# Optimization experiments

Measured on AMD Instinct MI355X. Metric: run time of the kernel, lower is better.

The kernel has to match this reference:

```python
import jax, jax.numpy as jnp
import numpy as np
from jax import lax

C = 24        # per-cell state channels
HID = 64      # update MLP hidden width
FIRE_RATE = 0.5
STEPS = 32


def _perception_kernel():
    # identity, sobel-x, sobel-y -> depthwise kernel (3C, 1, 3, 3) in OIHW,
    # tiled C times exactly like torch's kernel.repeat(c,1,1,1) with groups=c.
    ident = np.zeros((3, 3), np.float32); ident[1, 1] = 1.0
    sx = np.array([[-1, 0, 1], [-2, 0, 2], [-1, 0, 1]], np.float32) / 8.0
    sy = sx.T.copy()
    k = np.stack([ident, sx, sy])[:, None, :, :]   # (3, 1, 3, 3)
    return jnp.asarray(np.tile(k, (C, 1, 1, 1)))   # (3C, 1, 3, 3)


def setup_inputs() -> dict:
    key = jax.random.key(0)
    k0, k1, k2, k3 = jax.random.split(key, 4)
    B, H, W = 4, 128, 128
    state = jax.random.normal(k0, (B, C, H, W), jnp.float32)
    # scaled so 32 residual steps stay numerically tame (zero-init in the
    # original is a training trick that would make delta identically 0)
    w1 = jax.random.normal(k1, (HID, 3 * C), jnp.float32) * 0.1
    b1 = jnp.zeros((HID,), jnp.float32)
    w2 = jax.random.normal(k2, (C, HID), jnp.float32) * 0.01
    b2 = jnp.zeros((C,), jnp.float32)
    masks = jax.random.uniform(k3, (STEPS, B, 1, H, W), jnp.float32)
    return {"state": state, "w1": w1, "b1": b1, "w2": w2, "b2": b2, "masks": masks}


def reference(state, w1, b1, w2, b2, masks):
    kernel = _perception_kernel()

    def step(s, m):
        # grouped 3x3 depthwise perception: (B,C,H,W) -> (B,3C,H,W)
        p = lax.conv_general_dilated(
            s, kernel, window_strides=(1, 1), padding="SAME",
            feature_group_count=C,
            dimension_numbers=("NCHW", "OIHW", "NCHW"))
        # 1x1 conv MLP (pointwise, expressed as einsum over channels)
        h = jax.nn.relu(jnp.einsum("bchw,oc->bohw", p, w1) + b1[None, :, None, None])
        delta = jnp.einsum("bchw,oc->bohw", h, w2) + b2[None, :, None, None]
        # stochastic fire: update only cells where uniform < fire_rate
        fire = (m < FIRE_RATE).astype(s.dtype)
        return s + delta * fire, None

    out, _ = lax.scan(step, state, masks)
    return out
```

## Files before the change

### kernel.cpp

```cpp
#include <hip/hip_runtime.h>

typedef __bf16 bf16x8 __attribute__((ext_vector_type(8)));
typedef float  f32x4  __attribute__((ext_vector_type(4)));
typedef float  f32x2  __attribute__((ext_vector_type(2)));

#define NCH 24
#define CP  26
#define HW 128
#define IMG (HW*HW)
#define CHIMG (NCH*IMG)
#define SXP 20
#define SYP 8
#define S1XP 18
#define S1YP 6
#define S1N (S1XP*S1YP)

#define PW1_OFF ((size_t)(4*CHIMG)*4)
#define PW2_OFF (PW1_OFF + 12*64*8*2)
#define PB2_OFF (PW2_OFF + 4*64*8*2)

__global__ void nca_pack_weights(const float* __restrict__ w1, const float* __restrict__ b1,
                                 const float* __restrict__ w2, const float* __restrict__ b2,
                                 char* __restrict__ ws)
{
    short* pw1 = (short*)(ws + PW1_OFF);
    short* pw2 = (short*)(ws + PW2_OFF);
    float* pb2 = (float*)(ws + PB2_OFF);
    const int tid = threadIdx.x;
    for (int idx = tid; idx < 12*64*8; idx += 256) {
        int j  = idx & 7;
        int ll = (idx >> 3) & 63;
        int fs = idx >> 9;
        int m  = fs / 3, s = fs - 3*m;
        int row = m*16 + (ll & 15);
        int kp  = 32*s + 8*(ll >> 4) + j;
        int c = kp >> 2, tt = kp & 3;
        float v;
        if (tt < 3) v = w1[row*72 + 3*c + tt];
        else        v = (c == 0) ? b1[row] : 0.f;
        pw1[idx] = (short)__builtin_bit_cast(unsigned short, (__bf16)v);
    }
    for (int idx = tid; idx < 4*64*8; idx += 256) {
        int j  = idx & 7;
        int ll = (idx >> 3) & 63;
        int fs = idx >> 9;
        int m2 = fs >> 1, s2 = fs & 1;
        int row = m2*16 + (ll & 15);
        int h   = 32*s2 + 8*(ll >> 4) + j;
        float v = (row < 24) ? w2[row*64 + h] : 0.f;
        pw2[idx] = (short)__builtin_bit_cast(unsigned short, (__bf16)v);
    }
    for (int idx = tid; idx < 2*64*4; idx += 256) {
        int r  = idx & 3;
        int ll = (idx >> 2) & 63;
        int m2 = idx >> 8;
        int o  = m2*16 + 4*(ll >> 4) + r;
        pb2[idx] = (o < 24) ? b2[o] : 0.f;
    }
}

template<int XP>
__device__ __forceinline__ void nca_mlp(
    const float* __restrict__ stsrc, int sy, int sx,
    int l, int px, int g, int wv, short (*Hb)[16][72],
    const bf16x8 (&w1r)[12], const short* __restrict__ pw2,
    f32x4& d0, f32x4& d1)
{
    const float* base = stsrc + ((sy-1)*XP + (sx-1))*CP + 2*g;
    bf16x8 pf[3];
    #pragma unroll
    for (int s = 0; s < 3; ++s) {
        #define LDV(dy,dx) (*(const f32x2*)(base + ((dy)*XP + (dx))*CP + 8*s))
        f32x2 v00=LDV(0,0), v01=LDV(0,1), v02=LDV(0,2);
        f32x2 v10=LDV(1,0), v11=LDV(1,1), v12=LDV(1,2);
        f32x2 v20=LDV(2,0), v21=LDV(2,1), v22=LDV(2,2);
        #undef LDV
        f32x2 gx = (v02 - v00 + 2.f*(v12 - v10) + (v22 - v20)) * 0.125f;
        f32x2 gy = (v20 - v00 + 2.f*(v21 - v01) + (v22 - v02)) * 0.125f;
        pf[s][0] = (__bf16)v11.x;
        pf[s][1] = (__bf16)gx.x;
        pf[s][2] = (__bf16)gy.x;
        pf[s][3] = (__bf16)((s == 0 && g == 0) ? 1.f : 0.f);
        pf[s][4] = (__bf16)v11.y;
        pf[s][5] = (__bf16)gx.y;
        pf[s][6] = (__bf16)gy.y;
        pf[s][7] = (__bf16)0.f;
    }

    f32x4 acc1[4] = {};
    #pragma unroll
    for (int m = 0; m < 4; ++m) {
        #pragma unroll
        for (int s = 0; s < 3; ++s) {
            acc1[m] = __builtin_amdgcn_mfma_f32_16x16x32_bf16(w1r[m*3 + s], pf[s], acc1[m], 0, 0, 0);
        }
    }

    #pragma unroll
    for (int m = 0; m < 4; ++m) {
        unsigned int b0 = __builtin_bit_cast(unsigned short, (__bf16)fmaxf(acc1[m][0], 0.f));
        unsigned int b1_ = __builtin_bit_cast(unsigned short, (__bf16)fmaxf(acc1[m][1], 0.f));
        unsigned int b2_ = __builtin_bit_cast(unsigned short, (__bf16)fmaxf(acc1[m][2], 0.f));
        unsigned int b3 = __builtin_bit_cast(unsigned short, (__bf16)fmaxf(acc1[m][3], 0.f));
        uint2 w; w.x = b0 | (b1_ << 16); w.y = b2_ | (b3 << 16);
        *(uint2*)&Hb[wv][px][m*16 + 4*g] = w;
    }

    f32x4 acc2[2] = {};
    #pragma unroll
    for (int s2 = 0; s2 < 2; ++s2) {
        bf16x8 hv = *(const bf16x8*)&Hb[wv][px][8*g + 32*s2];
        #pragma unroll
        for (int m2 = 0; m2 < 2; ++m2) {
            bf16x8 a2 = *(const bf16x8*)&pw2[((m2*2 + s2)*64 + l)*8];
            acc2[m2] = __builtin_amdgcn_mfma_f32_16x16x32_bf16(a2, hv, acc2[m2], 0, 0, 0);
        }
    }
    d0 = acc2[0];
    d1 = acc2[1];
}

__global__ __launch_bounds__(256, 4) void nca_step2(
    const float* __restrict__ src, float* __restrict__ dst,
    const char* __restrict__ wsp, const float* __restrict__ masks, int step0)
{
    __shared__ __align__(16) float st_in[SYP*SXP*CP];
    __shared__ __align__(16) float st1[S1YP*S1XP*CP];
    __shared__ __align__(16) short Hb[4][16][72];

    const short* __restrict__ pw1 = (const short*)(wsp + PW1_OFF);
    const short* __restrict__ pw2 = (const short*)(wsp + PW2_OFF);
    const float* __restrict__ pb2 = (const float*)(wsp + PB2_OFF);

    const int tid = threadIdx.x;
    const int wv  = tid >> 6;
    const int l   = tid & 63;
    const int px  = l & 15;
    const int g   = l >> 4;

    bf16x8 w1r[12];
    #pragma unroll
    for (int i = 0; i < 12; ++i)
        w1r[i] = *(const bf16x8*)&pw1[(i*64 + l)*8];

    const int bid = blockIdx.x;
    const int t   = (bid & 7) * 128 + (bid >> 3);
    const int b   = t >> 8;
    const int y0  = ((t >> 3) & 31) * 4;
    const int x0  = (t & 7) * 16;

    const float* sb = src + b * CHIMG;
    for (int idx = tid; idx < NCH*SYP*SXP; idx += 256) {
        int xx = idx % SXP;
        int tt = idx / SXP;
        int yy = tt % SYP;
        int c  = tt / SYP;
        int gy = y0 + yy - 2;
        int gx = x0 + xx - 2;
        float v = 0.f;
        if ((unsigned)gy < (unsigned)HW && (unsigned)gx < (unsigned)HW)
            v = sb[c*IMG + gy*HW + gx];
        st_in[(yy*SXP + xx)*CP + c] = v;
    }
    __syncthreads();

    const float* mask1 = masks + ((size_t)step0*4 + b)*IMG;
    const float* mask2 = masks + ((size_t)(step0+1)*4 + b)*IMG;
    f32x4 b2v0 = *(const f32x4*)&pb2[(0*64 + l)*4];
    f32x4 b2v1 = *(const f32x4*)&pb2[(1*64 + l)*4];
    const f32x2 b2p0 = {b2v0[0], b2v0[1]}, b2p1 = {b2v0[2], b2v0[3]};
    const f32x2 b2p2 = {b2v1[0], b2v1[1]}, b2p3 = {b2v1[2], b2v1[3]};

    for (int itg = 0; itg < 2; ++itg) {
        const int slot = itg*4 + wv;
        if (slot*16 >= S1N) break;
        const int q  = slot*16 + px;
        const bool lane_valid = (q < S1N);
        const int qq = lane_valid ? q : 0;
        const int r1 = qq / S1XP;
        const int c1 = qq - r1*S1XP;

        f32x4 d0, d1;
        nca_mlp<SXP>(st_in, r1+1, c1+1, l, px, g, wv, Hb, w1r, pw2, d0, d1);

        const int gy = y0 + r1 - 1;
        const int gx = x0 + c1 - 1;
        const bool inimg = (unsigned)gy < (unsigned)HW && (unsigned)gx < (unsigned)HW;
        const int cy = inimg ? gy : 0;
        const int cx = inimg ? gx : 0;
        float mval = mask1[cy*HW + cx];
        float fire = (inimg && mval < 0.5f) ? 1.f : 0.f;
        float keep = inimg ? 1.f : 0.f;
        if (lane_valid) {
            const int pc  = ((r1+1)*SXP + (c1+1))*CP;
            const int pd  = (r1*S1XP + c1)*CP;
            f32x2 ra = *(const f32x2*)&st_in[pc + 4*g];
            f32x2 rb = *(const f32x2*)&st_in[pc + 4*g + 2];
            f32x2 t0 = {d0[0], d0[1]}, t1 = {d0[2], d0[3]};
            *(f32x2*)&st1[pd + 4*g]     = (ra + (t0 + b2p0) * fire) * keep;
            *(f32x2*)&st1[pd + 4*g + 2] = (rb + (t1 + b2p1) * fire) * keep;
            if (g < 2) {
                f32x2 rc = *(const f32x2*)&st_in[pc + 16 + 4*g];
                f32x2 rd = *(const f32x2*)&st_in[pc + 16 + 4*g + 2];
                f32x2 t2 = {d1[0], d1[1]}, t3 = {d1[2], d1[3]};
                *(f32x2*)&st1[pd + 16 + 4*g]     = (rc + (t2 + b2p2) * fire) * keep;
                *(f32x2*)&st1[pd + 16 + 4*g + 2] = (rd + (t3 + b2p3) * fire) * keep;
            }
        }
    }
    __syncthreads();

    {
        f32x4 d0, d1;
        nca_mlp<S1XP>(st1, wv+1, px+1, l, px, g, wv, Hb, w1r, pw2, d0, d1);

        const int x = x0 + px;
        const int y = y0 + wv;
        float mval = mask2[y*HW + x];
        float fire = (mval < 0.5f) ? 1.f : 0.f;
        const int pc = ((wv+1)*S1XP + (px+1))*CP;
        float* ob = dst + b*CHIMG + y*HW + x;

        f32x2 ra = *(const f32x2*)&st1[pc + 4*g];
        f32x2 rb = *(const f32x2*)&st1[pc + 4*g + 2];
        f32x2 t0 = {d0[0], d0[1]}, t1 = {d0[2], d0[3]};
        f32x2 o0 = ra + (t0 + b2p0) * fire;
        f32x2 o1 = rb + (t1 + b2p1) * fire;
        ob[(4*g + 0)*IMG] = o0.x;
        ob[(4*g + 1)*IMG] = o0.y;
        ob[(4*g + 2)*IMG] = o1.x;
        ob[(4*g + 3)*IMG] = o1.y;
        if (g < 2) {
            f32x2 rc = *(const f32x2*)&st1[pc + 16 + 4*g];
            f32x2 rd = *(const f32x2*)&st1[pc + 16 + 4*g + 2];
            f32x2 t2 = {d1[0], d1[1]}, t3 = {d1[2], d1[3]};
            f32x2 o2 = rc + (t2 + b2p2) * fire;
            f32x2 o3 = rd + (t3 + b2p3) * fire;
            ob[(16 + 4*g + 0)*IMG] = o2.x;
            ob[(16 + 4*g + 1)*IMG] = o2.y;
            ob[(16 + 4*g + 2)*IMG] = o3.x;
            ob[(16 + 4*g + 3)*IMG] = o3.y;
        }
    }
}

extern "C" void kernel_launch(void* const* d_in, const int* in_sizes, int n_in,
                              void* d_out, int out_size, void* d_ws, size_t ws_size,
                              hipStream_t stream) {
    const float* state = (const float*)d_in[0];
    const float* w1    = (const float*)d_in[1];
    const float* b1    = (const float*)d_in[2];
    const float* w2    = (const float*)d_in[3];
    const float* b2    = (const float*)d_in[4];
    const float* masks = (const float*)d_in[5];

    float* out = (float*)d_out;
    float* ws  = (float*)d_ws;
    const char* wsc = (const char*)d_ws;

    nca_pack_weights<<<dim3(1), dim3(256), 0, stream>>>(w1, b1, w2, b2, (char*)d_ws);

    for (int i = 0; i < 16; ++i) {
        const float* src = (i == 0) ? state : ((i & 1) ? ws : out);
        float*       dst = (i & 1) ? out : ws;
        nca_step2<<<dim3(1024), dim3(256), 0, stream>>>(src, dst, wsc, masks, 2*i);
    }
}
```

Measured before the change: 216.2 us.

## Enlarge fused two-step tiles to 8 rows with 512-thread blocks

Each block now covers a 16x8 output tile with 8 waves instead of 16x4 with 4 waves. This cuts the redundant halo recomputation of the intermediate step from 6 rows per 4 to 10 rows per 8, and reduces halo loads. The global-to-LDS staging loop is rewritten so each thread owns one channel/column and walks down the rows, replacing per-element div/mod. Shared memory per block and register pressure under launch_bounds(512,4) both grow, and the 12 first-stage slots spread unevenly over 8 waves.

```diff
diff --git a/kernel.cpp b/kernel.cpp
--- a/kernel.cpp
+++ b/kernel.cpp
@@ -10,10 +10,11 @@
 #define IMG (HW*HW)
 #define CHIMG (NCH*IMG)
 #define SXP 20
-#define SYP 8
+#define SYP 12
 #define S1XP 18
-#define S1YP 6
+#define S1YP 10
 #define S1N (S1XP*S1YP)
+#define NW 8
 
 #define PW1_OFF ((size_t)(4*CHIMG)*4)
 #define PW2_OFF (PW1_OFF + 12*64*8*2)
@@ -62,7 +63,7 @@
 template<int XP>
 __device__ __forceinline__ void nca_mlp(
     const float* __restrict__ stsrc, int sy, int sx,
-    int l, int px, int g, int wv, short (*Hb)[16][72],
+    int l, int px, int g, short (*hbw)[72],
     const bf16x8 (&w1r)[12], const short* __restrict__ pw2,
     f32x4& d0, f32x4& d1)
 {
@@ -103,13 +104,13 @@
         unsigned int b2_ = __builtin_bit_cast(unsigned short, (__bf16)fmaxf(acc1[m][2], 0.f));
         unsigned int b3 = __builtin_bit_cast(unsigned short, (__bf16)fmaxf(acc1[m][3], 0.f));
         uint2 w; w.x = b0 | (b1_ << 16); w.y = b2_ | (b3 << 16);
-        *(uint2*)&Hb[wv][px][m*16 + 4*g] = w;
+        *(uint2*)&hbw[px][m*16 + 4*g] = w;
     }
 
     f32x4 acc2[2] = {};
     #pragma unroll
     for (int s2 = 0; s2 < 2; ++s2) {
-        bf16x8 hv = *(const bf16x8*)&Hb[wv][px][8*g + 32*s2];
+        bf16x8 hv = *(const bf16x8*)&hbw[px][8*g + 32*s2];
         #pragma unroll
         for (int m2 = 0; m2 < 2; ++m2) {
             bf16x8 a2 = *(const bf16x8*)&pw2[((m2*2 + s2)*64 + l)*8];
@@ -120,13 +121,13 @@
     d1 = acc2[1];
 }
 
-__global__ __launch_bounds__(256, 4) void nca_step2(
+__global__ __launch_bounds__(512, 4) void nca_step2(
     const float* __restrict__ src, float* __restrict__ dst,
     const char* __restrict__ wsp, const float* __restrict__ masks, int step0)
 {
     __shared__ __align__(16) float st_in[SYP*SXP*CP];
     __shared__ __align__(16) float st1[S1YP*S1XP*CP];
-    __shared__ __align__(16) short Hb[4][16][72];
+    __shared__ __align__(16) short Hb[NW][16][72];
 
     const short* __restrict__ pw1 = (const short*)(wsp + PW1_OFF);
     const short* __restrict__ pw2 = (const short*)(wsp + PW2_OFF);
@@ -144,23 +145,27 @@
         w1r[i] = *(const bf16x8*)&pw1[(i*64 + l)*8];
 
     const int bid = blockIdx.x;
-    const int t   = (bid & 7) * 128 + (bid >> 3);
-    const int b   = t >> 8;
-    const int y0  = ((t >> 3) & 31) * 4;
-    const int x0  = (t & 7) * 16;
+    const int t   = (bid & 7) * 64 + (bid >> 3);
+    const int b   = t >> 7;
+    const int rem = t & 127;
+    const int y0  = (rem >> 3) * 8;
+    const int x0  = (rem & 7) * 16;
 
     const float* sb = src + b * CHIMG;
-    for (int idx = tid; idx < NCH*SYP*SXP; idx += 256) {
-        int xx = idx % SXP;
-        int tt = idx / SXP;
-        int yy = tt % SYP;
-        int c  = tt / SYP;
-        int gy = y0 + yy - 2;
-        int gx = x0 + xx - 2;
-        float v = 0.f;
-        if ((unsigned)gy < (unsigned)HW && (unsigned)gx < (unsigned)HW)
-            v = sb[c*IMG + gy*HW + gx];
-        st_in[(yy*SXP + xx)*CP + c] = v;
+    if (tid < 480) {
+        const int c  = tid / 20;
+        const int x  = tid - c*20;
+        const int gx = x0 + x - 2;
+        const bool vx = (unsigned)gx < (unsigned)HW;
+        const float* gp = sb + c*IMG + (y0 - 2)*HW + gx;
+        float* lp = &st_in[x*CP + c];
+        int gy = y0 - 2;
+        #pragma unroll
+        for (int yy = 0; yy < SYP; ++yy) {
+            bool v = vx && ((unsigned)gy < (unsigned)HW);
+            lp[yy*SXP*CP] = v ? gp[yy*HW] : 0.f;
+            ++gy;
+        }
     }
     __syncthreads();
 
@@ -171,40 +176,42 @@
     const f32x2 b2p0 = {b2v0[0], b2v0[1]}, b2p1 = {b2v0[2], b2v0[3]};
     const f32x2 b2p2 = {b2v1[0], b2v1[1]}, b2p3 = {b2v1[2], b2v1[3]};
 
-    for (int itg = 0; itg < 2; ++itg) {
-        const int slot = itg*4 + wv;
-        if (slot*16 >= S1N) break;
-        const int q  = slot*16 + px;
-        const bool lane_valid = (q < S1N);
-        const int qq = lane_valid ? q : 0;
-        const int r1 = qq / S1XP;
-        const int c1 = qq - r1*S1XP;
-
-        f32x4 d0, d1;
-        nca_mlp<SXP>(st_in, r1+1, c1+1, l, px, g, wv, Hb, w1r, pw2, d0, d1);
-
-        const int gy = y0 + r1 - 1;
-        const int gx = x0 + c1 - 1;
-        const bool inimg = (unsigned)gy < (unsigned)HW && (unsigned)gx < (unsigned)HW;
-        const int cy = inimg ? gy : 0;
-        const int cx = inimg ? gx : 0;
-        float mval = mask1[cy*HW + cx];
-        float fire = (inimg && mval < 0.5f) ? 1.f : 0.f;
-        float keep = inimg ? 1.f : 0.f;
-        if (lane_valid) {
-            const int pc  = ((r1+1)*SXP + (c1+1))*CP;
-            const int pd  = (r1*S1XP + c1)*CP;
-            f32x2 ra = *(const f32x2*)&st_in[pc + 4*g];
-            f32x2 rb = *(const f32x2*)&st_in[pc + 4*g + 2];
-            f32x2 t0 = {d0[0], d0[1]}, t1 = {d0[2], d0[3]};
-            *(f32x2*)&st1[pd + 4*g]     = (ra + (t0 + b2p0) * fire) * keep;
-            *(f32x2*)&st1[pd + 4*g + 2] = (rb + (t1 + b2p1) * fire) * keep;
-            if (g < 2) {
-                f32x2 rc = *(const f32x2*)&st_in[pc + 16 + 4*g];
-                f32x2 rd = *(const f32x2*)&st_in[pc + 16 + 4*g + 2];
-                f32x2 t2 = {d1[0], d1[1]}, t3 = {d1[2], d1[3]};
-                *(f32x2*)&st1[pd + 16 + 4*g]     = (rc + (t2 + b2p2) * fire) * keep;
-                *(f32x2*)&st1[pd + 16 + 4*g + 2] = (rd + (t3 + b2p3) * fire) * keep;
+    #pragma unroll
+    for (int it = 0; it < 2; ++it) {
+        const int slot = it*NW + wv;
+        if (slot < 12) {
+            const int q  = slot*16 + px;
+            const bool lane_valid = (q < S1N);
+            const int qq = lane_valid ? q : 0;
+            const int r1 = qq / S1XP;
+            const int c1 = qq - r1*S1XP;
+
+            f32x4 d0, d1;
+            nca_mlp<SXP>(st_in, r1+1, c1+1, l, px, g, Hb[wv], w1r, pw2, d0, d1);
+
+            const int gy = y0 + r1 - 1;
+            const int gx = x0 + c1 - 1;
+            const bool inimg = (unsigned)gy < (unsigned)HW && (unsigned)gx < (unsigned)HW;
+            const int cy = inimg ? gy : 0;
+            const int cx = inimg ? gx : 0;
+            float mval = mask1[cy*HW + cx];
+            float fire = (inimg && mval < 0.5f) ? 1.f : 0.f;
+            float keep = inimg ? 1.f : 0.f;
+            if (lane_valid) {
+                const int pc = ((r1+1)*SXP + (c1+1))*CP;
+                const int pd = (r1*S1XP + c1)*CP;
+                f32x2 ra = *(const f32x2*)&st_in[pc + 4*g];
+                f32x2 rb = *(const f32x2*)&st_in[pc + 4*g + 2];
+                f32x2 t0 = {d0[0], d0[1]}, t1 = {d0[2], d0[3]};
+                *(f32x2*)&st1[pd + 4*g]     = (ra + (t0 + b2p0) * fire) * keep;
+                *(f32x2*)&st1[pd + 4*g + 2] = (rb + (t1 + b2p1) * fire) * keep;
+                if (g < 2) {
+                    f32x2 rc = *(const f32x2*)&st_in[pc + 16 + 4*g];
+                    f32x2 rd = *(const f32x2*)&st_in[pc + 16 + 4*g + 2];
+                    f32x2 t2 = {d1[0], d1[1]}, t3 = {d1[2], d1[3]};
+                    *(f32x2*)&st1[pd + 16 + 4*g]     = (rc + (t2 + b2p2) * fire) * keep;
+                    *(f32x2*)&st1[pd + 16 + 4*g + 2] = (rd + (t3 + b2p3) * fire) * keep;
+                }
             }
         }
     }
@@ -212,7 +219,7 @@
 
     {
         f32x4 d0, d1;
-        nca_mlp<S1XP>(st1, wv+1, px+1, l, px, g, wv, Hb, w1r, pw2, d0, d1);
+        nca_mlp<S1XP>(st1, wv+1, px+1, l, px, g, Hb[wv], w1r, pw2, d0, d1);
 
         const int x = x0 + px;
         const int y = y0 + wv;
@@ -263,6 +270,6 @@
     for (int i = 0; i < 16; ++i) {
         const float* src = (i == 0) ? state : ((i & 1) ? ws : out);
         float*       dst = (i & 1) ? out : ws;
-        nca_step2<<<dim3(1024), dim3(256), 0, stream>>>(src, dst, wsc, masks, 2*i);
-    }
-}
+        nca_step2<<<dim3(512), dim3(512), 0, stream>>>(src, dst, wsc, masks, 2*i);
+    }
+}
```

Result: faster. 175.3 us (-18.9%).
